# Kernel tuning notes

Hardware: AMD Instinct MI355X
Metric: run time of the kernel (lower is better)

Reference implementation:

```python
import jax, jax.numpy as jnp
from jax import lax
import numpy as np

B, E, D, V, NB, R = 512, 128, 8, 50000, 4, 3  # batch, embed/hidden/classes, capsule_length, num_items, num_beh, routing iters
TP, TC, TF, TK = 50, 50, 50, 200  # purchase/cart/fav/click lengths


def setup_inputs() -> dict:
    key = jax.random.key(0)
    k = jax.random.split(key, 12)
    item_emb = jax.random.normal(k[4], (V + 1, E), jnp.float32)
    item_emb = item_emb.at[0].set(0.0)  # padding_idx=0
    return {
        "purchase_seq": jax.random.randint(k[0], (B, TP), 0, V + 1),
        "cart_seq": jax.random.randint(k[1], (B, TC), 0, V + 1),
        "fav_seq": jax.random.randint(k[2], (B, TF), 0, V + 1),
        "click_seq": jax.random.randint(k[3], (B, TK), 0, V + 1),
        "item_emb": item_emb,
        "gru_Wih": 0.1 * jax.random.normal(k[5], (NB, 3 * E, E), jnp.float32),
        "gru_Whh": 0.1 * jax.random.normal(k[6], (NB, 3 * E, E), jnp.float32),
        "gru_bih": jnp.zeros((NB, 3 * E), jnp.float32),
        "gru_bhh": jnp.zeros((NB, 3 * E), jnp.float32),
        "W": 0.01 * jax.random.uniform(k[7], (E, NB, E, D), dtype=jnp.float32),
        "w_scale": jnp.ones((E,), jnp.float32),
        "bias_vec": jnp.zeros((E,), jnp.float32),
        "alpha": jnp.full((1,), float(E), jnp.float32),
        "W_coef": 0.1 * jax.random.normal(k[8], (E, E + D, D), jnp.float32),
    }


def _gru_last(x, Wih, Whh, bih, bhh):
    """Standard GRU over x: (B, T, E); returns final hidden state (B, H)."""
    H = Whh.shape[1]

    def step(h, xt):
        gi = xt @ Wih.T + bih
        gh = h @ Whh.T + bhh
        ir, iz, inn = jnp.split(gi, 3, axis=-1)
        hr, hz, hn = jnp.split(gh, 3, axis=-1)
        r = jax.nn.sigmoid(ir + hr)
        z = jax.nn.sigmoid(iz + hz)
        n = jnp.tanh(inn + r * hn)
        return (1.0 - z) * n + z * h, None

    h0 = jnp.zeros((x.shape[0], H), x.dtype)
    h, _ = lax.scan(step, h0, jnp.swapaxes(x, 0, 1))
    return h


def _forward(seqs, item_emb, gru_Wih, gru_Whh, gru_bih, gru_bhh, W, w_scale, bias_vec, alpha, W_coef):
    hs = []
    for i, s in enumerate(seqs):  # fixed small loop over num_beh=4 structurally distinct GRUs
        emb = item_emb[s] * (s != 0)[..., None].astype(item_emb.dtype)
        hs.append(_gru_last(emb, gru_Wih[i], gru_Whh[i], gru_bih[i], gru_bhh[i]))
    e = jnp.stack(hs, axis=-1)  # (B, H, NB)  == stack(dim=1).permute(0,2,1)
    u = jnp.einsum('bht,htcd->bhcd', e, W)  # (B, H, C, D)
    b = jnp.zeros(u.shape[:3] + (1,), u.dtype)
    u_det = lax.stop_gradient(u)
    E_det = lax.stop_gradient(item_emb)
    for _ in range(R - 1):  # detached routing-by-agreement iterations
        c = jax.nn.softmax(b, axis=2)
        v = lax.stop_gradient(alpha) * jnp.sum(c * u_det, axis=1)  # (B, C, D)
        v_ = jnp.linalg.norm(v, axis=-1) * lax.stop_gradient(w_scale) + lax.stop_gradient(bias_vec)  # (B, C)
        p = jax.nn.softmax(v_ @ E_det.T, axis=-1) @ E_det  # (B, E) soft vocab lookup
        p = jnp.broadcast_to(p[:, None, :], (p.shape[0], u.shape[2], p.shape[-1]))  # (B, C, E)
        coef = jnp.einsum('bcd,cdD->bcD', jnp.concatenate([p, v], axis=-1), W_coef)  # (B, C, D)
        b = b + jnp.sum(u_det * coef[:, None], axis=-1, keepdims=True)
    c = jax.nn.softmax(b, axis=2)
    v = alpha * jnp.sum(c * u, axis=1)
    v_ = jnp.linalg.norm(v, axis=-1) * w_scale + bias_vec
    return v_ @ item_emb.T  # (B, V+1)


def reference(purchase_seq, cart_seq, fav_seq, click_seq, item_emb, gru_Wih, gru_Whh, gru_bih, gru_bhh, W, w_scale, bias_vec, alpha, W_coef):
    return _forward((purchase_seq, cart_seq, fav_seq, click_seq), item_emb, gru_Wih, gru_Whh,
                    gru_bih, gru_bhh, W, w_scale, bias_vec, alpha, W_coef)
```

## Files before the change

kernel.cpp:

```cpp
#include <hip/hip_runtime.h>
#include <math.h>

typedef __attribute__((ext_vector_type(8))) short bf16x8;
typedef __attribute__((ext_vector_type(4))) float f32x4;
typedef __attribute__((ext_vector_type(2))) float f32x2;
typedef __attribute__((ext_vector_type(4))) unsigned short u16x4;
typedef __attribute__((ext_vector_type(2))) _Float16 f16x2;
typedef __attribute__((ext_vector_type(4))) _Float16 f16x4;
typedef __attribute__((ext_vector_type(8))) _Float16 f16x8;

static __device__ __forceinline__ short f2bf(float f) {
  unsigned u = __builtin_bit_cast(unsigned, f);
  u += 0x7fffu + ((u >> 16) & 1u);
  return (short)(u >> 16);
}
static __device__ __forceinline__ float bf2f(unsigned short s) {
  unsigned u = ((unsigned)s) << 16;
  return __builtin_bit_cast(float, u);
}
static __device__ __forceinline__ f32x4 mfma16(bf16x8 a, bf16x8 b, f32x4 c) {
  return __builtin_amdgcn_mfma_f32_16x16x32_bf16(a, b, c, 0, 0, 0);
}
static __device__ __forceinline__ bf16x8 pack8v(f32x4 a, f32x4 b) {
  bf16x8 r;
  r[0]=f2bf(a[0]); r[1]=f2bf(a[1]); r[2]=f2bf(a[2]); r[3]=f2bf(a[3]);
  r[4]=f2bf(b[0]); r[5]=f2bf(b[1]); r[6]=f2bf(b[2]); r[7]=f2bf(b[3]);
  return r;
}
static __device__ __forceinline__ float fastrcp(float x) {
  float r;
  asm("v_rcp_f32_e32 %0, %1" : "=v"(r) : "v"(x));
  return r;
}
static __device__ __forceinline__ float dot4(f32x4 a, f32x4 b) {
  return a[0]*b[0] + a[1]*b[1] + a[2]*b[2] + a[3]*b[3];
}

#define LGKM_BARRIER() do {                                   \
    asm volatile("s_waitcnt lgkmcnt(0)" ::: "memory");        \
    __builtin_amdgcn_s_barrier();                             \
    __builtin_amdgcn_sched_barrier(0);                        \
  } while (0)

__global__ __launch_bounds__(512) void gi_gemm_kernel(
    const int* __restrict__ seq0, const int* __restrict__ seq1,
    const int* __restrict__ seq2, const int* __restrict__ seq3,
    const float* __restrict__ item_emb, const float* __restrict__ Wih,
    unsigned short* __restrict__ gi_t50, unsigned short* __restrict__ gi_click)
{
  const int b = blockIdx.x;
  int beh, tile0;
  if (b < 100)      { beh = 0; tile0 = b * 16; }
  else if (b < 200) { beh = 1; tile0 = (b - 100) * 16; }
  else if (b < 300) { beh = 2; tile0 = (b - 200) * 16; }
  else              { beh = 3; tile0 = (b - 300) * 16; }
  const int T = (beh == 3) ? 200 : 50;
  const int* seq = (beh == 0) ? seq0 : (beh == 1) ? seq1 : (beh == 2) ? seq2 : seq3;
  unsigned short* gibase = (beh == 3) ? gi_click : (gi_t50 + (size_t)beh * 9830400);

  const int tid = threadIdx.x;
  const int wave = tid >> 6, lane = tid & 63, lrow = lane & 15, lk8 = lane >> 4;
  const int bcol = wave * 16 + lrow;

  bf16x8 wif[3][4];
  const float* WihB = Wih + (size_t)beh * 384 * 128;
#pragma unroll
  for (int g = 0; g < 3; ++g) {
    const int wr = g * 128 + bcol;
#pragma unroll
    for (int kt = 0; kt < 4; ++kt) {
      const int k0 = kt * 32 + lk8 * 8;
      f32x4 a0 = *(const f32x4*)(WihB + (size_t)wr * 128 + k0);
      f32x4 a1 = *(const f32x4*)(WihB + (size_t)wr * 128 + k0 + 4);
      wif[g][kt] = pack8v(a0, a1);
    }
  }

  __shared__ short xt[16][132];
  const int gj = tid >> 5;
  const int gc = (tid & 31) * 4;

  for (int ti = 0; ti < 16; ++ti) {
    const int tile = tile0 + ti;
    const int r0blk = tile / T;
    const int t = tile - r0blk * T;
    {
      const int sidx = seq[(size_t)(r0blk * 16 + gj) * T + t];
      const f32x4 xv = *(const f32x4*)(item_emb + (size_t)sidx * 128 + gc);
      xt[gj][gc]     = f2bf(xv[0]);
      xt[gj][gc + 1] = f2bf(xv[1]);
      xt[gj][gc + 2] = f2bf(xv[2]);
      xt[gj][gc + 3] = f2bf(xv[3]);
    }
    __syncthreads();
    bf16x8 ax[4];
#pragma unroll
    for (int kt = 0; kt < 4; ++kt)
      ax[kt] = *(const bf16x8*)&xt[lrow][kt * 32 + lk8 * 8];
    f32x4 acc[3] = {{0,0,0,0},{0,0,0,0},{0,0,0,0}};
#pragma unroll
    for (int kt = 0; kt < 4; ++kt) {
      acc[0] = mfma16(ax[kt], wif[0][kt], acc[0]);
      acc[1] = mfma16(ax[kt], wif[1][kt], acc[1]);
      acc[2] = mfma16(ax[kt], wif[2][kt], acc[2]);
    }
    unsigned short* base = gibase + ((size_t)(r0blk * 4 + lk8) * T + t) * 1536;
    unsigned short* dst = base + bcol * 4;
#pragma unroll
    for (int g = 0; g < 3; ++g) {
      u16x4 o;
      o[0] = (unsigned short)f2bf(acc[g][0]);
      o[1] = (unsigned short)f2bf(acc[g][1]);
      o[2] = (unsigned short)f2bf(acc[g][2]);
      o[3] = (unsigned short)f2bf(acc[g][3]);
      *(u16x4*)(dst + g * 512) = o;
    }
    __syncthreads();
  }
}

__global__ __launch_bounds__(256, 2) void gru_rec5w_kernel(
    const float* __restrict__ Whh, const float* __restrict__ bih,
    const float* __restrict__ bhh,
    const unsigned short* __restrict__ gi_t50,
    const unsigned short* __restrict__ gi_click,
    const float* __restrict__ item_emb, short* __restrict__ Et,
    float* __restrict__ e_out)
{
  __shared__ short h0[16][140];
  __shared__ short h1[16][140];
  __shared__ float ttile[64][36];
  const int tid = threadIdx.x;

  if (blockIdx.x >= 512) {
    const int wb = blockIdx.x - 512;
    for (int unit = wb; unit < 3128; unit += 128) {
      const int vt = unit >> 2, kp = unit & 3;
      const int v0 = vt * 64, ks = kp * 32;
      const int r = tid >> 2, cc = (tid & 3) * 8;
      f32x4 x0 = {0,0,0,0}, x1 = {0,0,0,0};
      if (v0 + r < 50001) {
        x0 = *(const f32x4*)(item_emb + (size_t)(v0 + r) * 128 + ks + cc);
        x1 = *(const f32x4*)(item_emb + (size_t)(v0 + r) * 128 + ks + cc + 4);
      }
      *(f32x4*)&ttile[r][cc] = x0;
      *(f32x4*)&ttile[r][cc + 4] = x1;
      __syncthreads();
      const int k = tid >> 3, vs = (tid & 7) * 8;
#pragma unroll
      for (int j = 0; j < 8; j += 4) {
        u16x4 o;
        o[0] = (unsigned short)f2bf(ttile[vs + j][k]);
        o[1] = (unsigned short)f2bf(ttile[vs + j + 1][k]);
        o[2] = (unsigned short)f2bf(ttile[vs + j + 2][k]);
        o[3] = (unsigned short)f2bf(ttile[vs + j + 3][k]);
        *(u16x4*)((unsigned short*)Et + (size_t)(ks + k) * 50048 + v0 + vs + j) = o;
      }
      __syncthreads();
    }
    return;
  }

  const int beh = blockIdx.x >> 7;
  const int qt = blockIdx.x & 127;
  const int T = (beh == 3) ? 200 : 50;
  const unsigned short* gib =
      ((beh == 3) ? gi_click : (gi_t50 + (size_t)beh * 9830400)) + (size_t)qt * T * 1536;

  const int w = tid >> 6;
  const int lane = tid & 63;
  const int lrow = lane & 15;
  const int lk8 = lane >> 4;
  const int col0 = w * 32 + lrow;
  const int col1 = col0 + 16;

  bf16x8 whf[3][2][4];
  const float* WhhB = Whh + (size_t)beh * 384 * 128;
#pragma unroll
  for (int g = 0; g < 3; ++g) {
#pragma unroll
    for (int ct = 0; ct < 2; ++ct) {
      const int wr = g * 128 + (ct ? col1 : col0);
#pragma unroll
      for (int kt = 0; kt < 4; ++kt) {
        const int k0 = kt * 32 + lk8 * 8;
        f32x4 b0 = *(const f32x4*)(WhhB + (size_t)wr * 128 + k0);
        f32x4 b1 = *(const f32x4*)(WhhB + (size_t)wr * 128 + k0 + 4);
        whf[g][ct][kt] = pack8v(b0, b1);
      }
    }
  }
  float bR[2], bZ[2], bN[2], bHN[2];
#pragma unroll
  for (int ct = 0; ct < 2; ++ct) {
    const int c = ct ? col1 : col0;
    bR[ct]  = bih[beh * 384 + c] + bhh[beh * 384 + c];
    bZ[ct]  = bih[beh * 384 + 128 + c] + bhh[beh * 384 + 128 + c];
    bN[ct]  = bih[beh * 384 + 256 + c];
    bHN[ct] = bhh[beh * 384 + 256 + c];
  }

  for (int i = tid; i < 16 * 140; i += 256) { ((short*)h0)[i] = 0; ((short*)h1)[i] = 0; }
  float hreg[2] = {0.f, 0.f};
  __syncthreads();

  const unsigned short* gp0 = gib + col0 * 4 + lk8;
  const unsigned short* gp1 = gib + col1 * 4 + lk8;

  unsigned short ga[30], gb[30];

#define LOAD_CHUNK(BUF, C0) do {                                              \
    _Pragma("unroll")                                                         \
    for (int _s = 0; _s < 5; ++_s) {                                          \
      const size_t _o = (size_t)((C0) + _s) * 1536;                           \
      _Pragma("unroll")                                                       \
      for (int _g = 0; _g < 3; ++_g) {                                        \
        BUF[_s * 6 + 0 * 3 + _g] = gp0[_o + _g * 512];                        \
        BUF[_s * 6 + 1 * 3 + _g] = gp1[_o + _g * 512];                        \
      }                                                                       \
    }                                                                         \
  } while (0)

  short (*hin)[140] = h0;
  short (*hout)[140] = h1;

#define STEP(BUF, S) do {                                                     \
    bf16x8 ah[4];                                                             \
    _Pragma("unroll")                                                         \
    for (int kt = 0; kt < 4; ++kt)                                            \
      ah[kt] = *(const bf16x8*)&hin[lrow][kt * 32 + lk8 * 8];                 \
    f32x4 hr_[2], hz_[2], hn_[2];                                             \
    _Pragma("unroll")                                                         \
    for (int ct = 0; ct < 2; ++ct) {                                          \
      hr_[ct] = (f32x4){0,0,0,0}; hz_[ct] = (f32x4){0,0,0,0}; hn_[ct] = (f32x4){0,0,0,0}; \
      _Pragma("unroll")                                                       \
      for (int kt = 0; kt < 4; ++kt) {                                        \
        hr_[ct] = mfma16(ah[kt], whf[0][ct][kt], hr_[ct]);                    \
        hz_[ct] = mfma16(ah[kt], whf[1][ct][kt], hz_[ct]);                    \
        hn_[ct] = mfma16(ah[kt], whf[2][ct][kt], hn_[ct]);                    \
      }                                                                       \
    }                                                                         \
    _Pragma("unroll")                                                         \
    for (int ct = 0; ct < 2; ++ct) {                                          \
      const float xr = bf2f(BUF[(S)*6 + ct*3 + 0]) + bR[ct] + hr_[ct][0];     \
      const float xz = bf2f(BUF[(S)*6 + ct*3 + 1]) + bZ[ct] + hz_[ct][0];     \
      const float ea = __expf(-xr);                                           \
      const float eb = __expf(-xz);                                           \
      const float pa = 1.f + ea, pb = 1.f + eb;                               \
      const float rd = fastrcp(pa * pb);                                      \
      const float rr = pb * rd;                                               \
      const float zz = pa * rd;                                               \
      const float tn = bf2f(BUF[(S)*6 + ct*3 + 2]) + bN[ct] + rr * (hn_[ct][0] + bHN[ct]); \
      const float tt = __expf(-2.f * tn);                                     \
      const float nn = (1.f - tt) * fastrcp(1.f + tt);                        \
      hreg[ct] = nn + zz * (hreg[ct] - nn);                                   \
      hout[lk8 * 4][ct ? col1 : col0] = f2bf(hreg[ct]);                       \
    }                                                                         \
    LGKM_BARRIER();                                                           \
    short (*_tmp)[140] = hin; hin = hout; hout = _tmp;                        \
  } while (0)

  LOAD_CHUNK(ga, 0);
  for (int c = 0; c < T; c += 10) {
    if (c + 5 < T) LOAD_CHUNK(gb, c + 5);
    STEP(ga, 0); STEP(ga, 1); STEP(ga, 2); STEP(ga, 3); STEP(ga, 4);
    if (c + 10 < T) LOAD_CHUNK(ga, c + 10);
    STEP(gb, 0); STEP(gb, 1); STEP(gb, 2); STEP(gb, 3); STEP(gb, 4);
  }
#undef STEP
#undef LOAD_CHUNK

#pragma unroll
  for (int ct = 0; ct < 2; ++ct)
    e_out[(size_t)(qt * 4 + lk8) * 512 + (ct ? col1 : col0) * 4 + beh] = hreg[ct];
}

template<int MODE>
__global__ __launch_bounds__(256, 1) void route_kernel(
    const _Float16* __restrict__ b_old, _Float16* __restrict__ b_new,
    const float* __restrict__ e_buf, const float* __restrict__ W,
    const float* __restrict__ coef_buf,
    const float* __restrict__ w_scale, const float* __restrict__ bias_vec,
    const float* __restrict__ alpha,
    float* __restrict__ v_buf, float* __restrict__ vn_buf)
{
  __shared__ float e_lds[4][128][4];
  __shared__ float vacc[4][4][128][8];
  const int g0 = blockIdx.x * 4;
  const int tid = threadIdx.x;
  const int wv = tid >> 6, ln = tid & 63;
  const int c0 = ln * 2;
  for (int i = tid; i < 2048; i += 256) ((float*)e_lds)[i] = e_buf[(size_t)g0 * 512 + i];

  f32x4 cf[4][2][2];
  if (MODE != 0) {
#pragma unroll
    for (int g = 0; g < 4; ++g)
#pragma unroll
      for (int cc = 0; cc < 2; ++cc) {
        cf[g][cc][0] = *(const f32x4*)(coef_buf + (size_t)(g0 + g) * 1024 + (c0 + cc) * 8);
        cf[g][cc][1] = *(const f32x4*)(coef_buf + (size_t)(g0 + g) * 1024 + (c0 + cc) * 8 + 4);
      }
  }
  __syncthreads();

  f32x4 av[4][2][2];
#pragma unroll
  for (int g = 0; g < 4; ++g)
#pragma unroll
    for (int cc = 0; cc < 2; ++cc) { av[g][cc][0] = (f32x4){0,0,0,0}; av[g][cc][1] = (f32x4){0,0,0,0}; }

  const int hbeg = wv * 32;
  for (int h = hbeg; h < hbeg + 32; ++h) {
    f32x4 wr[4][2][2];
#pragma unroll
    for (int t = 0; t < 4; ++t) {
      const float* wp = W + ((size_t)(h * 4 + t) * 128 + c0) * 8;
      wr[t][0][0] = *(const f32x4*)(wp);
      wr[t][0][1] = *(const f32x4*)(wp + 4);
      wr[t][1][0] = *(const f32x4*)(wp + 8);
      wr[t][1][1] = *(const f32x4*)(wp + 12);
    }
    f16x2 bo[4];
    if (MODE == 2) {
#pragma unroll
      for (int g = 0; g < 4; ++g)
        bo[g] = *(const f16x2*)(b_old + (size_t)(g0 + g) * 16384 + h * 128 + c0);
    }
#pragma unroll
    for (int g = 0; g < 4; ++g) {
      const f32x4 ev = *(const f32x4*)&e_lds[g][h][0];
      f32x4 u[2][2];
#pragma unroll
      for (int cc = 0; cc < 2; ++cc)
#pragma unroll
        for (int dd = 0; dd < 2; ++dd)
          u[cc][dd] = ev[0]*wr[0][cc][dd] + ev[1]*wr[1][cc][dd]
                    + ev[2]*wr[2][cc][dd] + ev[3]*wr[3][cc][dd];
      float cv0, cv1;
      if (MODE == 0) {
        cv0 = 0.0078125f; cv1 = 0.0078125f;
      } else {
        float b0 = dot4(u[0][0], cf[g][0][0]) + dot4(u[0][1], cf[g][0][1]);
        float b1 = dot4(u[1][0], cf[g][1][0]) + dot4(u[1][1], cf[g][1][1]);
        if (MODE == 2) { b0 += (float)bo[g][0]; b1 += (float)bo[g][1]; }
        if (MODE == 1) {
          f16x2 bw; bw[0] = (_Float16)b0; bw[1] = (_Float16)b1;
          *(f16x2*)(b_new + (size_t)(g0 + g) * 16384 + h * 128 + c0) = bw;
        }
        float m = fmaxf(b0, b1);
#pragma unroll
        for (int off = 32; off > 0; off >>= 1) m = fmaxf(m, __shfl_xor(m, off));
        const float e0 = __expf(b0 - m), e1 = __expf(b1 - m);
        float s = e0 + e1;
#pragma unroll
        for (int off = 32; off > 0; off >>= 1) s += __shfl_xor(s, off);
        const float inv = 1.f / s;
        cv0 = e0 * inv; cv1 = e1 * inv;
      }
      av[g][0][0] += cv0 * u[0][0]; av[g][0][1] += cv0 * u[0][1];
      av[g][1][0] += cv1 * u[1][0]; av[g][1][1] += cv1 * u[1][1];
    }
  }
#pragma unroll
  for (int g = 0; g < 4; ++g)
#pragma unroll
    for (int cc = 0; cc < 2; ++cc) {
      *(f32x4*)&vacc[wv][g][c0 + cc][0] = av[g][cc][0];
      *(f32x4*)&vacc[wv][g][c0 + cc][4] = av[g][cc][1];
    }
  __syncthreads();

  const float al = alpha[0];
  const int rg = tid >> 6;
  const int rc = (tid & 63) * 2;
#pragma unroll
  for (int cc = 0; cc < 2; ++cc) {
    const int c = rc + cc;
    f32x4 s0 = *(const f32x4*)&vacc[0][rg][c][0];
    f32x4 s1 = *(const f32x4*)&vacc[0][rg][c][4];
#pragma unroll
    for (int wq = 1; wq < 4; ++wq) {
      s0 += *(const f32x4*)&vacc[wq][rg][c][0];
      s1 += *(const f32x4*)&vacc[wq][rg][c][4];
    }
    s0 *= al; s1 *= al;
    *(f32x4*)(v_buf + (size_t)(g0 + rg) * 1024 + c * 8) = s0;
    *(f32x4*)(v_buf + (size_t)(g0 + rg) * 1024 + c * 8 + 4) = s1;
    const float ss = dot4(s0, s0) + dot4(s1, s1);
    vn_buf[(g0 + rg) * 128 + c] = sqrtf(ss) * w_scale[c] + bias_vec[c];
  }
}

__global__ __launch_bounds__(512) void logits16s_kernel(
    const float* __restrict__ vn, const float* __restrict__ E,
    _Float16* __restrict__ out16, float* __restrict__ pm, float* __restrict__ ps)
{
  __shared__ short et[64][136];
  const int n0 = blockIdx.x * 64;
  const int tid = threadIdx.x;
  const int wave = tid >> 6, lane = tid & 63, lrow = lane & 15, lk8 = lane >> 4;
  {
    const int r = tid >> 3, ks = (tid & 7) * 16;
    const int v = n0 + r;
    f32x4 a = {0,0,0,0}, b = {0,0,0,0}, c = {0,0,0,0}, d = {0,0,0,0};
    if (v < 50001) {
      const float* p = E + (size_t)v * 128 + ks;
      a = *(const f32x4*)p; b = *(const f32x4*)(p + 4);
      c = *(const f32x4*)(p + 8); d = *(const f32x4*)(p + 12);
    }
    *(bf16x8*)&et[r][ks] = pack8v(a, b);
    *(bf16x8*)&et[r][ks + 8] = pack8v(c, d);
  }
  __syncthreads();
  for (int mb = 0; mb < 4; ++mb) {
    const int m0 = mb * 128;
    const int arow = m0 + wave * 16 + lrow;
    bf16x8 afr[4];
#pragma unroll
    for (int kt = 0; kt < 4; ++kt) {
      const float* p = vn + (size_t)arow * 128 + kt * 32 + lk8 * 8;
      afr[kt] = pack8v(*(const f32x4*)p, *(const f32x4*)(p + 4));
    }
    f32x4 acc[4] = {{0,0,0,0},{0,0,0,0},{0,0,0,0},{0,0,0,0}};
#pragma unroll
    for (int kt = 0; kt < 4; ++kt) {
#pragma unroll
      for (int nt = 0; nt < 4; ++nt) {
        const bf16x8 bfr = *(const bf16x8*)&et[nt * 16 + lrow][kt * 32 + lk8 * 8];
        acc[nt] = mfma16(afr[kt], bfr, acc[nt]);
      }
    }
    float xv[4][4];
#pragma unroll
    for (int nt = 0; nt < 4; ++nt) {
      const int col = n0 + nt * 16 + lrow;
      const int row = m0 + wave * 16 + lk8 * 4;
#pragma unroll
      for (int e2 = 0; e2 < 4; ++e2) {
        const float v = (col < 50001) ? acc[nt][e2] : -60000.f;
        const _Float16 h16 = (_Float16)v;
        out16[(size_t)(row + e2) * 50048 + col] = h16;
        xv[e2][nt] = (float)h16;
      }
    }
#pragma unroll
    for (int e2 = 0; e2 < 4; ++e2) {
      float lm = fmaxf(fmaxf(xv[e2][0], xv[e2][1]), fmaxf(xv[e2][2], xv[e2][3]));
#pragma unroll
      for (int off = 8; off > 0; off >>= 1) lm = fmaxf(lm, __shfl_xor(lm, off));
      float s = __expf(xv[e2][0] - lm) + __expf(xv[e2][1] - lm)
              + __expf(xv[e2][2] - lm) + __expf(xv[e2][3] - lm);
#pragma unroll
      for (int off = 8; off > 0; off >>= 1) s += __shfl_xor(s, off);
      if (lrow == 0) {
        const int row = m0 + wave * 16 + lk8 * 4 + e2;
        pm[(size_t)row * 784 + blockIdx.x] = lm;
        ps[(size_t)row * 784 + blockIdx.x] = s;
      }
    }
  }
}

__global__ __launch_bounds__(256) void rowstats_p_kernel(
    const float* __restrict__ pm, const float* __restrict__ ps,
    float* __restrict__ row_m, float* __restrict__ row_inv, float* __restrict__ p_buf)
{
  const int b = blockIdx.x;
  const int tid = threadIdx.x;
  if (tid < 128) p_buf[b * 128 + tid] = 0.f;
  const float* pmr = pm + (size_t)b * 784;
  const float* psr = ps + (size_t)b * 784;
  __shared__ float sm[4], ssum[4];
  const int wv = tid >> 6, ln = tid & 63;
  float m = -1e30f;
  for (int i = tid; i < 782; i += 256) m = fmaxf(m, pmr[i]);
#pragma unroll
  for (int off = 32; off > 0; off >>= 1) m = fmaxf(m, __shfl_xor(m, off));
  if (ln == 0) sm[wv] = m;
  __syncthreads();
  const float M = fmaxf(fmaxf(sm[0], sm[1]), fmaxf(sm[2], sm[3]));
  float s = 0.f;
  for (int i = tid; i < 782; i += 256) s += psr[i] * __expf(pmr[i] - M);
#pragma unroll
  for (int off = 32; off > 0; off >>= 1) s += __shfl_xor(s, off);
  if (ln == 0) ssum[wv] = s;
  __syncthreads();
  if (tid == 0) {
    row_m[b] = M;
    row_inv[b] = 1.f / (ssum[0] + ssum[1] + ssum[2] + ssum[3]);
  }
}

__global__ __launch_bounds__(256) void pgemm16_kernel(
    const _Float16* __restrict__ lg, const short* __restrict__ Et,
    const float* __restrict__ row_m, const float* __restrict__ row_inv,
    float* __restrict__ p_buf)
{
  const int tid = threadIdx.x;
  const int wave = tid >> 6, lane = tid & 63, lrow = lane & 15, lk8 = lane >> 4;
  const int m0 = blockIdx.y * 64;
  const int row = m0 + wave * 16 + lrow;
  const float rm = row_m[row], ri = row_inv[row];
  const _Float16* lp = lg + (size_t)row * 50048;
  const int kbeg = blockIdx.x * 1024;
  const int kend = (kbeg + 1024 <= 50048) ? kbeg + 1024 : 50048;
  f32x4 acc[8] = {{0,0,0,0},{0,0,0,0},{0,0,0,0},{0,0,0,0},
                  {0,0,0,0},{0,0,0,0},{0,0,0,0},{0,0,0,0}};
  for (int v0 = kbeg; v0 < kend; v0 += 32) {
    const int kb = v0 + lk8 * 8;
    const f16x8 v8 = *(const f16x8*)(lp + kb);
    bf16x8 afr;
#pragma unroll
    for (int j = 0; j < 8; ++j) afr[j] = f2bf(__expf((float)v8[j] - rm) * ri);
#pragma unroll
    for (int nt = 0; nt < 8; ++nt) {
      const bf16x8 bfr = *(const bf16x8*)(Et + (size_t)(nt * 16 + lrow) * 50048 + kb);
      acc[nt] = mfma16(afr, bfr, acc[nt]);
    }
  }
#pragma unroll
  for (int nt = 0; nt < 8; ++nt)
#pragma unroll
    for (int e2 = 0; e2 < 4; ++e2)
      atomicAdd(&p_buf[(size_t)(m0 + wave * 16 + lk8 * 4 + e2) * 128 + nt * 16 + lrow], acc[nt][e2]);
}

__global__ __launch_bounds__(256) void coef_kernel(
    const float* __restrict__ p_buf, const float* __restrict__ v_buf,
    const float* __restrict__ W_coef, float* __restrict__ coef_buf)
{
  __shared__ float p_lds[4][128];
  const int g0 = blockIdx.x * 4;
  const int tid = threadIdx.x;
  for (int i = tid; i < 512; i += 256) ((float*)p_lds)[i] = p_buf[(size_t)g0 * 128 + i];
  __syncthreads();
  const int c = tid >> 1, dh = (tid & 1) * 4;
  float vg[4][8];
#pragma unroll
  for (int g = 0; g < 4; ++g) {
    const f32x4 va = *(const f32x4*)(v_buf + (size_t)(g0 + g) * 1024 + c * 8);
    const f32x4 vb = *(const f32x4*)(v_buf + (size_t)(g0 + g) * 1024 + c * 8 + 4);
    vg[g][0]=va[0]; vg[g][1]=va[1]; vg[g][2]=va[2]; vg[g][3]=va[3];
    vg[g][4]=vb[0]; vg[g][5]=vb[1]; vg[g][6]=vb[2]; vg[g][7]=vb[3];
  }
  const float* wc = W_coef + (size_t)c * 1088 + dh;
  f32x4 acc[4] = {{0,0,0,0},{0,0,0,0},{0,0,0,0},{0,0,0,0}};
  for (int dp = 0; dp < 128; ++dp) {
    const f32x4 w4 = *(const f32x4*)(wc + (size_t)dp * 8);
#pragma unroll
    for (int g = 0; g < 4; ++g) acc[g] += p_lds[g][dp] * w4;
  }
#pragma unroll
  for (int q = 0; q < 8; ++q) {
    const f32x4 w4 = *(const f32x4*)(wc + (size_t)(128 + q) * 8);
#pragma unroll
    for (int g = 0; g < 4; ++g) acc[g] += vg[g][q] * w4;
  }
#pragma unroll
  for (int g = 0; g < 4; ++g)
    *(f32x4*)(coef_buf + (size_t)(g0 + g) * 1024 + c * 8 + dh) = acc[g];
}

__global__ __launch_bounds__(512) void logits32_kernel(
    const float* __restrict__ vn, const float* __restrict__ E,
    float* __restrict__ out)
{
  __shared__ short et[64][136];
  const int n0 = blockIdx.x * 64;
  const int tid = threadIdx.x;
  const int wave = tid >> 6, lane = tid & 63, lrow = lane & 15, lk8 = lane >> 4;
  {
    const int r = tid >> 3, ks = (tid & 7) * 16;
    const int v = n0 + r;
    f32x4 a = {0,0,0,0}, b = {0,0,0,0}, c = {0,0,0,0}, d = {0,0,0,0};
    if (v < 50001) {
      const float* p = E + (size_t)v * 128 + ks;
      a = *(const f32x4*)p; b = *(const f32x4*)(p + 4);
      c = *(const f32x4*)(p + 8); d = *(const f32x4*)(p + 12);
    }
    *(bf16x8*)&et[r][ks] = pack8v(a, b);
    *(bf16x8*)&et[r][ks + 8] = pack8v(c, d);
  }
  __syncthreads();
  for (int mb = 0; mb < 4; ++mb) {
    const int m0 = mb * 128;
    const int arow = m0 + wave * 16 + lrow;
    bf16x8 afr[4];
#pragma unroll
    for (int kt = 0; kt < 4; ++kt) {
      const float* p = vn + (size_t)arow * 128 + kt * 32 + lk8 * 8;
      afr[kt] = pack8v(*(const f32x4*)p, *(const f32x4*)(p + 4));
    }
    f32x4 acc[4] = {{0,0,0,0},{0,0,0,0},{0,0,0,0},{0,0,0,0}};
#pragma unroll
    for (int kt = 0; kt < 4; ++kt) {
#pragma unroll
      for (int nt = 0; nt < 4; ++nt) {
        const bf16x8 bfr = *(const bf16x8*)&et[nt * 16 + lrow][kt * 32 + lk8 * 8];
        acc[nt] = mfma16(afr[kt], bfr, acc[nt]);
      }
    }
#pragma unroll
    for (int nt = 0; nt < 4; ++nt) {
      const int col = n0 + nt * 16 + lrow;
      if (col < 50001) {
        const int row = m0 + wave * 16 + lk8 * 4;
#pragma unroll
        for (int e2 = 0; e2 < 4; ++e2)
          out[(size_t)(row + e2) * 50001 + col] = acc[nt][e2];
      }
    }
  }
}

extern "C" void kernel_launch(void* const* d_in, const int* in_sizes, int n_in,
                              void* d_out, int out_size, void* d_ws, size_t ws_size,
                              hipStream_t stream) {
  const int* seq0 = (const int*)d_in[0];
  const int* seq1 = (const int*)d_in[1];
  const int* seq2 = (const int*)d_in[2];
  const int* seq3 = (const int*)d_in[3];
  const float* item_emb = (const float*)d_in[4];
  const float* Wih = (const float*)d_in[5];
  const float* Whh = (const float*)d_in[6];
  const float* bih = (const float*)d_in[7];
  const float* bhh = (const float*)d_in[8];
  const float* W = (const float*)d_in[9];
  const float* w_scale = (const float*)d_in[10];
  const float* bias_vec = (const float*)d_in[11];
  const float* alpha = (const float*)d_in[12];
  const float* W_coef = (const float*)d_in[13];
  float* out = (float*)d_out;
  _Float16* lg16 = (_Float16*)d_out;

  char* ws = (char*)d_ws;
  float* e_buf       = (float*)(ws);
  _Float16* b_state  = (_Float16*)(ws + 1048576);
  float* v_buf    = (float*)(ws + 34603008);
  float* vn_buf   = (float*)(ws + 36700160);
  float* p_buf    = (float*)(ws + 36962304);
  float* coef_buf = (float*)(ws + 37224448);
  float* row_m    = (float*)(ws + 39321600);
  float* row_inv  = (float*)(ws + 39323648);
  float* pstat_m  = (float*)(ws + 39325696);
  float* pstat_s  = (float*)(ws + 40931328);

  unsigned short* gi_t50   = (unsigned short*)(ws + 1048576);
  unsigned short* gi_click = (unsigned short*)d_out;
  short* Et = (short*)((char*)d_out + 78643200);

  gi_gemm_kernel<<<dim3(700), 512, 0, stream>>>(seq0, seq1, seq2, seq3, item_emb, Wih,
                                                gi_t50, gi_click);
  gru_rec5w_kernel<<<dim3(640), 256, 0, stream>>>(Whh, bih, bhh, gi_t50, gi_click,
                                                  item_emb, Et, e_buf);
  route_kernel<0><<<dim3(128), 256, 0, stream>>>(nullptr, nullptr, e_buf, W, nullptr,
                                                 w_scale, bias_vec, alpha, v_buf, vn_buf);
  logits16s_kernel<<<dim3(782), 512, 0, stream>>>(vn_buf, item_emb, lg16, pstat_m, pstat_s);
  rowstats_p_kernel<<<dim3(512), 256, 0, stream>>>(pstat_m, pstat_s, row_m, row_inv, p_buf);
  pgemm16_kernel<<<dim3(49, 8), 256, 0, stream>>>(lg16, Et, row_m, row_inv, p_buf);
  coef_kernel<<<dim3(128), 256, 0, stream>>>(p_buf, v_buf, W_coef, coef_buf);
  route_kernel<1><<<dim3(128), 256, 0, stream>>>(nullptr, b_state, e_buf, W, coef_buf,
                                                 w_scale, bias_vec, alpha, v_buf, vn_buf);
  logits16s_kernel<<<dim3(782), 512, 0, stream>>>(vn_buf, item_emb, lg16, pstat_m, pstat_s);
  rowstats_p_kernel<<<dim3(512), 256, 0, stream>>>(pstat_m, pstat_s, row_m, row_inv, p_buf);
  pgemm16_kernel<<<dim3(49, 8), 256, 0, stream>>>(lg16, Et, row_m, row_inv, p_buf);
  coef_kernel<<<dim3(128), 256, 0, stream>>>(p_buf, v_buf, W_coef, coef_buf);
  route_kernel<2><<<dim3(128), 256, 0, stream>>>(b_state, nullptr, e_buf, W, coef_buf,
                                                 w_scale, bias_vec, alpha, v_buf, vn_buf);
  logits32_kernel<<<dim3(782), 512, 0, stream>>>(vn_buf, item_emb, out);
}
```

Before: 787.5 us.

## Replace logits/rowstats/pgemm pipeline with split-K flash-style softmax-matmul kernel

Before, each routing iteration ran three kernels for the soft vocab lookup: logits16s wrote the full 512x50048 fp16 logits to memory, rowstats reduced the per-block max and sum, and pgemm16 re-read the logits to do exp and multiply by E. This is replaced by a flash-attention-style kernel with an online softmax. Each of 49 vocab chunks keeps a running max and sum plus a partial output, and combine_coef merges the partials before computing coef. The embedding-to-bf16 side job in the GRU kernel now writes E in its natural row layout instead of a transposed layout, and the flash kernel transposes each tile in LDS. This removes the large logits write/read and the atomics, at the cost of LDS transposes, extra syncs, and 49-way partial buffers.

```diff
diff --git a/kernel.cpp b/kernel.cpp
--- a/kernel.cpp
+++ b/kernel.cpp
@@ -6,8 +6,6 @@
 typedef __attribute__((ext_vector_type(2))) float f32x2;
 typedef __attribute__((ext_vector_type(4))) unsigned short u16x4;
 typedef __attribute__((ext_vector_type(2))) _Float16 f16x2;
-typedef __attribute__((ext_vector_type(4))) _Float16 f16x4;
-typedef __attribute__((ext_vector_type(8))) _Float16 f16x8;
 
 static __device__ __forceinline__ short f2bf(float f) {
   unsigned u = __builtin_bit_cast(unsigned, f);
@@ -124,39 +122,24 @@
     const float* __restrict__ bhh,
     const unsigned short* __restrict__ gi_t50,
     const unsigned short* __restrict__ gi_click,
-    const float* __restrict__ item_emb, short* __restrict__ Et,
+    const float* __restrict__ item_emb, unsigned short* __restrict__ Ebf,
     float* __restrict__ e_out)
 {
   __shared__ short h0[16][140];
   __shared__ short h1[16][140];
-  __shared__ float ttile[64][36];
   const int tid = threadIdx.x;
 
   if (blockIdx.x >= 512) {
     const int wb = blockIdx.x - 512;
-    for (int unit = wb; unit < 3128; unit += 128) {
-      const int vt = unit >> 2, kp = unit & 3;
-      const int v0 = vt * 64, ks = kp * 32;
-      const int r = tid >> 2, cc = (tid & 3) * 8;
-      f32x4 x0 = {0,0,0,0}, x1 = {0,0,0,0};
-      if (v0 + r < 50001) {
-        x0 = *(const f32x4*)(item_emb + (size_t)(v0 + r) * 128 + ks + cc);
-        x1 = *(const f32x4*)(item_emb + (size_t)(v0 + r) * 128 + ks + cc + 4);
-      }
-      *(f32x4*)&ttile[r][cc] = x0;
-      *(f32x4*)&ttile[r][cc + 4] = x1;
-      __syncthreads();
-      const int k = tid >> 3, vs = (tid & 7) * 8;
-#pragma unroll
-      for (int j = 0; j < 8; j += 4) {
-        u16x4 o;
-        o[0] = (unsigned short)f2bf(ttile[vs + j][k]);
-        o[1] = (unsigned short)f2bf(ttile[vs + j + 1][k]);
-        o[2] = (unsigned short)f2bf(ttile[vs + j + 2][k]);
-        o[3] = (unsigned short)f2bf(ttile[vs + j + 3][k]);
-        *(u16x4*)((unsigned short*)Et + (size_t)(ks + k) * 50048 + v0 + vs + j) = o;
-      }
-      __syncthreads();
+    for (size_t i8 = (size_t)(wb * 256 + tid) * 8; i8 < 50048u * 128u; i8 += 32768u * 8u) {
+      const int row = (int)(i8 >> 7);
+      bf16x8 o = {0,0,0,0,0,0,0,0};
+      if (row < 50001) {
+        const f32x4 a = *(const f32x4*)(item_emb + i8);
+        const f32x4 b = *(const f32x4*)(item_emb + i8 + 4);
+        o = pack8v(a, b);
+      }
+      *(bf16x8*)(Ebf + i8) = o;
     }
     return;
   }
@@ -392,148 +375,156 @@
   }
 }
 
-__global__ __launch_bounds__(512) void logits16s_kernel(
-    const float* __restrict__ vn, const float* __restrict__ E,
-    _Float16* __restrict__ out16, float* __restrict__ pm, float* __restrict__ ps)
+__global__ __launch_bounds__(256, 2) void flash_kernel(
+    const float* __restrict__ vn, const unsigned short* __restrict__ Ebf,
+    float* __restrict__ o_part, float* __restrict__ ms_part)
 {
-  __shared__ short et[64][136];
-  const int n0 = blockIdx.x * 64;
+  __shared__ short e_nat[64][136];
+  __shared__ short e_tr[128][72];
+  __shared__ short p_lds[4][16][72];
+  const int xc = blockIdx.x;
   const int tid = threadIdx.x;
-  const int wave = tid >> 6, lane = tid & 63, lrow = lane & 15, lk8 = lane >> 4;
-  {
-    const int r = tid >> 3, ks = (tid & 7) * 16;
-    const int v = n0 + r;
-    f32x4 a = {0,0,0,0}, b = {0,0,0,0}, c = {0,0,0,0}, d = {0,0,0,0};
-    if (v < 50001) {
-      const float* p = E + (size_t)v * 128 + ks;
-      a = *(const f32x4*)p; b = *(const f32x4*)(p + 4);
-      c = *(const f32x4*)(p + 8); d = *(const f32x4*)(p + 12);
-    }
-    *(bf16x8*)&et[r][ks] = pack8v(a, b);
-    *(bf16x8*)&et[r][ks + 8] = pack8v(c, d);
-  }
-  __syncthreads();
-  for (int mb = 0; mb < 4; ++mb) {
-    const int m0 = mb * 128;
-    const int arow = m0 + wave * 16 + lrow;
-    bf16x8 afr[4];
+  const int w = tid >> 6, lane = tid & 63, lrow = lane & 15, lk8 = lane >> 4;
+  const int rowbase = blockIdx.y * 64 + w * 16;
+
+  bf16x8 qf[4];
+#pragma unroll
+  for (int kt = 0; kt < 4; ++kt) {
+    const float* p = vn + (size_t)(rowbase + lrow) * 128 + kt * 32 + lk8 * 8;
+    qf[kt] = pack8v(*(const f32x4*)p, *(const f32x4*)(p + 4));
+  }
+
+  f32x4 o_acc[8] = {{0,0,0,0},{0,0,0,0},{0,0,0,0},{0,0,0,0},
+                    {0,0,0,0},{0,0,0,0},{0,0,0,0},{0,0,0,0}};
+  float m_run[4] = {-1e30f, -1e30f, -1e30f, -1e30f};
+  float s_run[4] = {0.f, 0.f, 0.f, 0.f};
+
+  const int kbeg = xc * 1024;
+  const int nst = (kbeg + 1024 <= 50048) ? 16 : (50048 - kbeg) / 64;
+  const int sr = tid >> 2, sseg = (tid & 3) * 32;
+
+  for (int st = 0; st < nst; ++st) {
+    const int v0 = kbeg + st * 64;
+    {
+      bf16x8 ev[4];
+#pragma unroll
+      for (int q = 0; q < 4; ++q)
+        ev[q] = *(const bf16x8*)(Ebf + (size_t)(v0 + sr) * 128 + sseg + q * 8);
+#pragma unroll
+      for (int q = 0; q < 4; ++q)
+        *(bf16x8*)&e_nat[sr][sseg + q * 8] = ev[q];
+#pragma unroll
+      for (int q = 0; q < 4; ++q)
+#pragma unroll
+        for (int j = 0; j < 8; ++j)
+          e_tr[sseg + q * 8 + j][sr] = ev[q][j];
+    }
+    __syncthreads();
+    f32x4 sacc[4] = {{0,0,0,0},{0,0,0,0},{0,0,0,0},{0,0,0,0}};
 #pragma unroll
     for (int kt = 0; kt < 4; ++kt) {
-      const float* p = vn + (size_t)arow * 128 + kt * 32 + lk8 * 8;
-      afr[kt] = pack8v(*(const f32x4*)p, *(const f32x4*)(p + 4));
-    }
-    f32x4 acc[4] = {{0,0,0,0},{0,0,0,0},{0,0,0,0},{0,0,0,0}};
-#pragma unroll
-    for (int kt = 0; kt < 4; ++kt) {
 #pragma unroll
       for (int nt = 0; nt < 4; ++nt) {
-        const bf16x8 bfr = *(const bf16x8*)&et[nt * 16 + lrow][kt * 32 + lk8 * 8];
-        acc[nt] = mfma16(afr[kt], bfr, acc[nt]);
-      }
-    }
-    float xv[4][4];
-#pragma unroll
-    for (int nt = 0; nt < 4; ++nt) {
-      const int col = n0 + nt * 16 + lrow;
-      const int row = m0 + wave * 16 + lk8 * 4;
-#pragma unroll
-      for (int e2 = 0; e2 < 4; ++e2) {
-        const float v = (col < 50001) ? acc[nt][e2] : -60000.f;
-        const _Float16 h16 = (_Float16)v;
-        out16[(size_t)(row + e2) * 50048 + col] = h16;
-        xv[e2][nt] = (float)h16;
-      }
+        const bf16x8 bfr = *(const bf16x8*)&e_nat[nt * 16 + lrow][kt * 32 + lk8 * 8];
+        sacc[nt] = mfma16(qf[kt], bfr, sacc[nt]);
+      }
+    }
+    if (v0 + 64 > 50001) {
+#pragma unroll
+      for (int nt = 0; nt < 4; ++nt)
+        if (v0 + nt * 16 + lrow >= 50001)
+          sacc[nt] = (f32x4){-1e30f, -1e30f, -1e30f, -1e30f};
     }
 #pragma unroll
     for (int e2 = 0; e2 < 4; ++e2) {
-      float lm = fmaxf(fmaxf(xv[e2][0], xv[e2][1]), fmaxf(xv[e2][2], xv[e2][3]));
-#pragma unroll
-      for (int off = 8; off > 0; off >>= 1) lm = fmaxf(lm, __shfl_xor(lm, off));
-      float s = __expf(xv[e2][0] - lm) + __expf(xv[e2][1] - lm)
-              + __expf(xv[e2][2] - lm) + __expf(xv[e2][3] - lm);
-#pragma unroll
-      for (int off = 8; off > 0; off >>= 1) s += __shfl_xor(s, off);
-      if (lrow == 0) {
-        const int row = m0 + wave * 16 + lk8 * 4 + e2;
-        pm[(size_t)row * 784 + blockIdx.x] = lm;
-        ps[(size_t)row * 784 + blockIdx.x] = s;
-      }
-    }
-  }
-}
-
-__global__ __launch_bounds__(256) void rowstats_p_kernel(
-    const float* __restrict__ pm, const float* __restrict__ ps,
-    float* __restrict__ row_m, float* __restrict__ row_inv, float* __restrict__ p_buf)
+      float mt = fmaxf(fmaxf(sacc[0][e2], sacc[1][e2]), fmaxf(sacc[2][e2], sacc[3][e2]));
+      mt = fmaxf(mt, __shfl_xor(mt, 1));
+      mt = fmaxf(mt, __shfl_xor(mt, 2));
+      mt = fmaxf(mt, __shfl_xor(mt, 4));
+      mt = fmaxf(mt, __shfl_xor(mt, 8));
+      const float mn = fmaxf(m_run[e2], mt);
+      const float scale = __expf(m_run[e2] - mn);
+      m_run[e2] = mn;
+      float pv[4];
+#pragma unroll
+      for (int nt = 0; nt < 4; ++nt) pv[nt] = __expf(sacc[nt][e2] - mn);
+      float ps = pv[0] + pv[1] + pv[2] + pv[3];
+      ps += __shfl_xor(ps, 1);
+      ps += __shfl_xor(ps, 2);
+      ps += __shfl_xor(ps, 4);
+      ps += __shfl_xor(ps, 8);
+      s_run[e2] = s_run[e2] * scale + ps;
+#pragma unroll
+      for (int nt8 = 0; nt8 < 8; ++nt8) o_acc[nt8][e2] *= scale;
+#pragma unroll
+      for (int nt = 0; nt < 4; ++nt)
+        p_lds[w][lk8 * 4 + e2][nt * 16 + lrow] = f2bf(pv[nt]);
+    }
+#pragma unroll
+    for (int kt2 = 0; kt2 < 2; ++kt2) {
+      const bf16x8 pa = *(const bf16x8*)&p_lds[w][lrow][kt2 * 32 + lk8 * 8];
+#pragma unroll
+      for (int nt8 = 0; nt8 < 8; ++nt8) {
+        const bf16x8 bfr = *(const bf16x8*)&e_tr[nt8 * 16 + lrow][kt2 * 32 + lk8 * 8];
+        o_acc[nt8] = mfma16(pa, bfr, o_acc[nt8]);
+      }
+    }
+    __syncthreads();
+  }
+
+#pragma unroll
+  for (int nt8 = 0; nt8 < 8; ++nt8)
+#pragma unroll
+    for (int e2 = 0; e2 < 4; ++e2)
+      o_part[((size_t)xc * 512 + rowbase + lk8 * 4 + e2) * 128 + nt8 * 16 + lrow] = o_acc[nt8][e2];
+  if (lrow == 0) {
+#pragma unroll
+    for (int e2 = 0; e2 < 4; ++e2) {
+      const int row = rowbase + lk8 * 4 + e2;
+      ms_part[((size_t)row * 49 + xc) * 2]     = m_run[e2];
+      ms_part[((size_t)row * 49 + xc) * 2 + 1] = s_run[e2];
+    }
+  }
+}
+
+__global__ __launch_bounds__(256) void combine_coef_kernel(
+    const float* __restrict__ o_part, const float* __restrict__ ms_part,
+    const float* __restrict__ v_buf, const float* __restrict__ W_coef,
+    float* __restrict__ coef_buf)
 {
-  const int b = blockIdx.x;
-  const int tid = threadIdx.x;
-  if (tid < 128) p_buf[b * 128 + tid] = 0.f;
-  const float* pmr = pm + (size_t)b * 784;
-  const float* psr = ps + (size_t)b * 784;
-  __shared__ float sm[4], ssum[4];
-  const int wv = tid >> 6, ln = tid & 63;
-  float m = -1e30f;
-  for (int i = tid; i < 782; i += 256) m = fmaxf(m, pmr[i]);
-#pragma unroll
-  for (int off = 32; off > 0; off >>= 1) m = fmaxf(m, __shfl_xor(m, off));
-  if (ln == 0) sm[wv] = m;
-  __syncthreads();
-  const float M = fmaxf(fmaxf(sm[0], sm[1]), fmaxf(sm[2], sm[3]));
-  float s = 0.f;
-  for (int i = tid; i < 782; i += 256) s += psr[i] * __expf(pmr[i] - M);
-#pragma unroll
-  for (int off = 32; off > 0; off >>= 1) s += __shfl_xor(s, off);
-  if (ln == 0) ssum[wv] = s;
-  __syncthreads();
-  if (tid == 0) {
-    row_m[b] = M;
-    row_inv[b] = 1.f / (ssum[0] + ssum[1] + ssum[2] + ssum[3]);
-  }
-}
-
-__global__ __launch_bounds__(256) void pgemm16_kernel(
-    const _Float16* __restrict__ lg, const short* __restrict__ Et,
-    const float* __restrict__ row_m, const float* __restrict__ row_inv,
-    float* __restrict__ p_buf)
-{
-  const int tid = threadIdx.x;
-  const int wave = tid >> 6, lane = tid & 63, lrow = lane & 15, lk8 = lane >> 4;
-  const int m0 = blockIdx.y * 64;
-  const int row = m0 + wave * 16 + lrow;
-  const float rm = row_m[row], ri = row_inv[row];
-  const _Float16* lp = lg + (size_t)row * 50048;
-  const int kbeg = blockIdx.x * 1024;
-  const int kend = (kbeg + 1024 <= 50048) ? kbeg + 1024 : 50048;
-  f32x4 acc[8] = {{0,0,0,0},{0,0,0,0},{0,0,0,0},{0,0,0,0},
-                  {0,0,0,0},{0,0,0,0},{0,0,0,0},{0,0,0,0}};
-  for (int v0 = kbeg; v0 < kend; v0 += 32) {
-    const int kb = v0 + lk8 * 8;
-    const f16x8 v8 = *(const f16x8*)(lp + kb);
-    bf16x8 afr;
-#pragma unroll
-    for (int j = 0; j < 8; ++j) afr[j] = f2bf(__expf((float)v8[j] - rm) * ri);
-#pragma unroll
-    for (int nt = 0; nt < 8; ++nt) {
-      const bf16x8 bfr = *(const bf16x8*)(Et + (size_t)(nt * 16 + lrow) * 50048 + kb);
-      acc[nt] = mfma16(afr, bfr, acc[nt]);
-    }
-  }
-#pragma unroll
-  for (int nt = 0; nt < 8; ++nt)
-#pragma unroll
-    for (int e2 = 0; e2 < 4; ++e2)
-      atomicAdd(&p_buf[(size_t)(m0 + wave * 16 + lk8 * 4 + e2) * 128 + nt * 16 + lrow], acc[nt][e2]);
-}
-
-__global__ __launch_bounds__(256) void coef_kernel(
-    const float* __restrict__ p_buf, const float* __restrict__ v_buf,
-    const float* __restrict__ W_coef, float* __restrict__ coef_buf)
-{
-  __shared__ float p_lds[4][128];
+  __shared__ float wg[4][64];
+  __shared__ float p_s[4][128];
   const int g0 = blockIdx.x * 4;
   const int tid = threadIdx.x;
-  for (int i = tid; i < 512; i += 256) ((float*)p_lds)[i] = p_buf[(size_t)g0 * 128 + i];
+  const int w = tid >> 6, lane = tid & 63;
+  {
+    const int row = g0 + w;
+    float ml = -1e30f, sl = 0.f;
+    if (lane < 49) {
+      ml = ms_part[((size_t)row * 49 + lane) * 2];
+      sl = ms_part[((size_t)row * 49 + lane) * 2 + 1];
+    }
+    float M = ml;
+#pragma unroll
+    for (int off = 32; off > 0; off >>= 1) M = fmaxf(M, __shfl_xor(M, off));
+    float e = (lane < 49) ? sl * __expf(ml - M) : 0.f;
+    float S = e;
+#pragma unroll
+    for (int off = 32; off > 0; off >>= 1) S += __shfl_xor(S, off);
+    const float inv = 1.f / S;
+    if (lane < 49) wg[w][lane] = __expf(ml - M) * inv;
+  }
+  __syncthreads();
+  {
+    const int d = tid & 127, gh = tid >> 7;
+    for (int gg = gh; gg < 4; gg += 2) {
+      const int row = g0 + gg;
+      float acc = 0.f;
+      for (int x = 0; x < 49; ++x)
+        acc += o_part[((size_t)x * 512 + row) * 128 + d] * wg[gg][x];
+      p_s[gg][d] = acc;
+    }
+  }
   __syncthreads();
   const int c = tid >> 1, dh = (tid & 1) * 4;
   float vg[4][8];
@@ -545,21 +536,21 @@
     vg[g][4]=vb[0]; vg[g][5]=vb[1]; vg[g][6]=vb[2]; vg[g][7]=vb[3];
   }
   const float* wc = W_coef + (size_t)c * 1088 + dh;
-  f32x4 acc[4] = {{0,0,0,0},{0,0,0,0},{0,0,0,0},{0,0,0,0}};
+  f32x4 acc4[4] = {{0,0,0,0},{0,0,0,0},{0,0,0,0},{0,0,0,0}};
   for (int dp = 0; dp < 128; ++dp) {
     const f32x4 w4 = *(const f32x4*)(wc + (size_t)dp * 8);
 #pragma unroll
-    for (int g = 0; g < 4; ++g) acc[g] += p_lds[g][dp] * w4;
+    for (int g = 0; g < 4; ++g) acc4[g] += p_s[g][dp] * w4;
   }
 #pragma unroll
   for (int q = 0; q < 8; ++q) {
     const f32x4 w4 = *(const f32x4*)(wc + (size_t)(128 + q) * 8);
 #pragma unroll
-    for (int g = 0; g < 4; ++g) acc[g] += vg[g][q] * w4;
+    for (int g = 0; g < 4; ++g) acc4[g] += vg[g][q] * w4;
   }
 #pragma unroll
   for (int g = 0; g < 4; ++g)
-    *(f32x4*)(coef_buf + (size_t)(g0 + g) * 1024 + c * 8 + dh) = acc[g];
+    *(f32x4*)(coef_buf + (size_t)(g0 + g) * 1024 + c * 8 + dh) = acc4[g];
 }
 
 __global__ __launch_bounds__(512) void logits32_kernel(
@@ -632,40 +623,32 @@
   const float* alpha = (const float*)d_in[12];
   const float* W_coef = (const float*)d_in[13];
   float* out = (float*)d_out;
-  _Float16* lg16 = (_Float16*)d_out;
 
   char* ws = (char*)d_ws;
   float* e_buf       = (float*)(ws);
   _Float16* b_state  = (_Float16*)(ws + 1048576);
   float* v_buf    = (float*)(ws + 34603008);
   float* vn_buf   = (float*)(ws + 36700160);
-  float* p_buf    = (float*)(ws + 36962304);
   float* coef_buf = (float*)(ws + 37224448);
-  float* row_m    = (float*)(ws + 39321600);
-  float* row_inv  = (float*)(ws + 39323648);
-  float* pstat_m  = (float*)(ws + 39325696);
-  float* pstat_s  = (float*)(ws + 40931328);
+  float* o_part   = (float*)(ws + 39325696);
+  float* ms_part  = (float*)(ws + 52170752);
 
   unsigned short* gi_t50   = (unsigned short*)(ws + 1048576);
   unsigned short* gi_click = (unsigned short*)d_out;
-  short* Et = (short*)((char*)d_out + 78643200);
+  unsigned short* Ebf = (unsigned short*)((char*)d_out + 78643200);
 
   gi_gemm_kernel<<<dim3(700), 512, 0, stream>>>(seq0, seq1, seq2, seq3, item_emb, Wih,
                                                 gi_t50, gi_click);
   gru_rec5w_kernel<<<dim3(640), 256, 0, stream>>>(Whh, bih, bhh, gi_t50, gi_click,
-                                                  item_emb, Et, e_buf);
+                                                  item_emb, Ebf, e_buf);
   route_kernel<0><<<dim3(128), 256, 0, stream>>>(nullptr, nullptr, e_buf, W, nullptr,
                                                  w_scale, bias_vec, alpha, v_buf, vn_buf);
-  logits16s_kernel<<<dim3(782), 512, 0, stream>>>(vn_buf, item_emb, lg16, pstat_m, pstat_s);
-  rowstats_p_kernel<<<dim3(512), 256, 0, stream>>>(pstat_m, pstat_s, row_m, row_inv, p_buf);
-  pgemm16_kernel<<<dim3(49, 8), 256, 0, stream>>>(lg16, Et, row_m, row_inv, p_buf);
-  coef_kernel<<<dim3(128), 256, 0, stream>>>(p_buf, v_buf, W_coef, coef_buf);
+  flash_kernel<<<dim3(49, 8), 256, 0, stream>>>(vn_buf, Ebf, o_part, ms_part);
+  combine_coef_kernel<<<dim3(128), 256, 0, stream>>>(o_part, ms_part, v_buf, W_coef, coef_buf);
   route_kernel<1><<<dim3(128), 256, 0, stream>>>(nullptr, b_state, e_buf, W, coef_buf,
                                                  w_scale, bias_vec, alpha, v_buf, vn_buf);
-  logits16s_kernel<<<dim3(782), 512, 0, stream>>>(vn_buf, item_emb, lg16, pstat_m, pstat_s);
-  rowstats_p_kernel<<<dim3(512), 256, 0, stream>>>(pstat_m, pstat_s, row_m, row_inv, p_buf);
-  pgemm16_kernel<<<dim3(49, 8), 256, 0, stream>>>(lg16, Et, row_m, row_inv, p_buf);
-  coef_kernel<<<dim3(128), 256, 0, stream>>>(p_buf, v_buf, W_coef, coef_buf);
+  flash_kernel<<<dim3(49, 8), 256, 0, stream>>>(vn_buf, Ebf, o_part, ms_part);
+  combine_coef_kernel<<<dim3(128), 256, 0, stream>>>(o_part, ms_part, v_buf, W_coef, coef_buf);
   route_kernel<2><<<dim3(128), 256, 0, stream>>>(b_state, nullptr, e_buf, W, coef_buf,
                                                  w_scale, bias_vec, alpha, v_buf, vn_buf);
   logits32_kernel<<<dim3(782), 512, 0, stream>>>(vn_buf, item_emb, out);
```

New measurement: 659.0 us. -16.3%, faster.
